# Kernel tuning notes

Hardware: AMD Instinct MI355X
Metric: run time of the kernel (lower is better)

Reference implementation:

```python
import jax, jax.numpy as jnp
import numpy as np

TOPK = 3
RAT_S = 0.05


def conv4d(x, w, bs):
    """Faithful fused version of the looped Conv4d (stride=1, padding=1, l_k=3).

    x:  (b, c_in, l, d, h, w)
    w:  (c_out, c_in, l_k, d_k, h_k, w_k)  -- w[:, :, i] is the i-th Conv3d weight
    bs: (l_k, c_out)                        -- per-i Conv3d biases
    The torch loop computes out[f] = sum_i conv3d_i(x[f + i - l_k//2]) for valid
    frame indices, which is exactly a 4D cross-correlation; the bias of conv3d_i
    is added once per VALID i, so boundary frames get fewer bias terms.
    """
    out = jax.lax.conv_general_dilated(
        x, w, window_strides=(1, 1, 1, 1), padding=[(1, 1)] * 4,
        dimension_numbers=("NCABXY", "OIABXY", "NCABXY"))
    l_i = x.shape[2]
    l_k = w.shape[2]
    f = jnp.arange(l_i)
    j = f[:, None] + jnp.arange(l_k)[None, :] - l_k // 2  # source frame per (f, i)
    valid = ((j >= 0) & (j < l_i)).astype(x.dtype)        # (l, l_k)
    bias = valid @ bs                                     # (l, c_out)
    return out + bias.T[None, :, :, None, None, None]


def zero_window(x_aff, h, w, rat_s):
    """x_aff: (b, h*w, h, w). Suppress a Gaussian window centered at each
    channel's (r, c) source location."""
    dt = x_aff.dtype
    sr = jnp.asarray(h * rat_s, dt)
    sc = jnp.asarray(w * rat_s, dt)
    ind_r = jnp.arange(h, dtype=dt)
    ind_c = jnp.arange(w, dtype=dt)
    cent_r = jnp.repeat(jnp.arange(h), w).astype(dt)  # (h*w,)
    cent_c = jnp.tile(jnp.arange(w), h).astype(dt)    # (h*w,)
    gr = jnp.exp(-((ind_r[None, :] - cent_r[:, None]) ** 2) / (2 * sr ** 2))  # (hw, h)
    gc = jnp.exp(-((ind_c[None, :] - cent_c[:, None]) ** 2) / (2 * sc ** 2))  # (hw, w)
    g = 1.0 - gr[:, :, None] * gc[:, None, :]  # (hw, h, w)
    return x_aff * g[None]


def setup_inputs() -> dict:
    key = jax.random.key(0)
    k = jax.random.split(key, 5)
    b, c, h, w = 4, 256, 32, 32
    x = jax.random.normal(k[0], (b, c, h, w), dtype=jnp.float32)
    w1 = jax.random.normal(k[1], (16, 1, 3, 3, 3, 3), dtype=jnp.float32) * 0.2
    b1 = jax.random.normal(k[2], (3, 16), dtype=jnp.float32) * 0.05
    w2 = jax.random.normal(k[3], (1, 16, 3, 3, 3, 3), dtype=jnp.float32) * 0.1
    b2 = jax.random.normal(k[4], (3, 1), dtype=jnp.float32) * 0.05
    return {"x": x, "w1": w1, "b1": b1, "w2": w2, "b2": b2}


def reference(x, w1, b1, w2, b2):
    b, c, h1, ww1 = x.shape
    n = h1 * ww1
    # F.normalize over channel dim (p=2, eps=1e-12)
    xn = x / jnp.maximum(jnp.linalg.norm(x, axis=1, keepdims=True), 1e-12)
    q = xn.transpose(0, 2, 3, 1).reshape(b, n, c)      # (b, hw, c)
    kmat = xn.reshape(b, c, n)                          # (b, c, hw)
    aff = jnp.einsum("bnc,bcm->bnm", q, kmat)          # (b, hw, hw)
    aff = zero_window(aff.reshape(b, n, h1, ww1), h1, ww1, RAT_S)
    x_fc = aff.reshape(b, 1, h1, ww1, h1, ww1)
    y = conv4d(x_fc, w1, b1)                            # (b, 16, h1, w1, h2, w2)
    y = conv4d(y, w2, b2)                               # (b, 1,  h1, w1, h2, w2)
    xc = y.reshape(b, n, h1, ww1)                       # (b, hw, h2, w2)
    # top-k values along dim=-3 (the query/channel axis)
    vals = jax.lax.top_k(xc.transpose(0, 2, 3, 1), TOPK)[0]  # (b, h2, w2, k)
    return vals.transpose(0, 3, 1, 2)                   # (b, k, h2, w2)
```

## Files before the change

kernel.cpp:

```cpp
#include <hip/hip_runtime.h>

#define HW 1024
#define CCH 256


typedef _Float16 h2v __attribute__((ext_vector_type(2)));
typedef short bf16x8 __attribute__((ext_vector_type(8)));
typedef float f32x4 __attribute__((ext_vector_type(4)));

__device__ __forceinline__ float fdot2(unsigned a, unsigned b, float c) {
#if __has_builtin(__builtin_amdgcn_fdot2)
    return __builtin_amdgcn_fdot2(__builtin_bit_cast(h2v, a),
                                  __builtin_bit_cast(h2v, b), c, false);
#else
    h2v ha = __builtin_bit_cast(h2v, a), hb = __builtin_bit_cast(h2v, b);
    return c + (float)ha.x * (float)hb.x + (float)ha.y * (float)hb.y;
#endif
}
__device__ __forceinline__ unsigned packh2(float x, float y) {
    h2v h;
    h.x = (_Float16)x;
    h.y = (_Float16)y;
    return __builtin_bit_cast(unsigned, h);
}
__device__ __forceinline__ unsigned short f2bf(float f) {
    unsigned u = __float_as_uint(f);
    u += 0x7fffu + ((u >> 16) & 1u);
    return (unsigned short)(u >> 16);
}

__global__ __launch_bounds__(256) void norm_kernel(const float* __restrict__ x,
                                                   unsigned short* __restrict__ xnT) {
    __shared__ float red[16][17];
    __shared__ float invs[16];
    int b = blockIdx.y;
    int p0 = blockIdx.x * 16;
    int cg = threadIdx.x >> 4;
    int pp = threadIdx.x & 15;
    int p = p0 + pp;
    const float* xb = x + (size_t)b * CCH * HW;
    float ss = 0.f;
#pragma unroll
    for (int i = 0; i < 16; ++i) {
        float v = xb[(size_t)(cg * 16 + i) * HW + p];
        ss += v * v;
    }
    red[cg][pp] = ss;
    __syncthreads();
    if (threadIdx.x < 16) {
        float s = 0.f;
#pragma unroll
        for (int g = 0; g < 16; ++g) s += red[g][threadIdx.x];
        invs[threadIdx.x] = 1.0f / fmaxf(sqrtf(s), 1e-12f);
    }
    __syncthreads();
    float inv = invs[pp];
    unsigned* o = (unsigned*)(xnT + ((size_t)b * HW + p) * CCH) + cg * 8;
#pragma unroll
    for (int i = 0; i < 8; ++i) {
        int c = cg * 16 + 2 * i;
        unsigned lo = f2bf(xb[(size_t)c * HW + p] * inv);
        unsigned hi = f2bf(xb[(size_t)(c + 1) * HW + p] * inv);
        o[i] = lo | (hi << 16);
    }
}

__global__ __launch_bounds__(256) void aff_kernel(const unsigned short* __restrict__ xnT,
                                                  unsigned short* __restrict__ Af16) {
    int b = blockIdx.z;
    int p0 = blockIdx.y * 64, m0 = blockIdx.x * 64;
    const unsigned short* X = xnT + (size_t)b * HW * CCH;
    int lane = threadIdx.x & 63, w = threadIdx.x >> 6;
    int pw = p0 + (w >> 1) * 32, mw = m0 + (w & 1) * 32;
    int lr = lane & 15, lg = lane >> 4;
    f32x4 acc[2][2] = {};
    for (int ks = 0; ks < 8; ++ks) {
        int kc = ks * 32 + lg * 8;
        bf16x8 a0 = *(const bf16x8*)&X[(size_t)(pw + lr) * CCH + kc];
        bf16x8 a1 = *(const bf16x8*)&X[(size_t)(pw + 16 + lr) * CCH + kc];
        bf16x8 b0 = *(const bf16x8*)&X[(size_t)(mw + lr) * CCH + kc];
        bf16x8 b1 = *(const bf16x8*)&X[(size_t)(mw + 16 + lr) * CCH + kc];
        acc[0][0] = __builtin_amdgcn_mfma_f32_16x16x32_bf16(a0, b0, acc[0][0], 0, 0, 0);
        acc[0][1] = __builtin_amdgcn_mfma_f32_16x16x32_bf16(a0, b1, acc[0][1], 0, 0, 0);
        acc[1][0] = __builtin_amdgcn_mfma_f32_16x16x32_bf16(a1, b0, acc[1][0], 0, 0, 0);
        acc[1][1] = __builtin_amdgcn_mfma_f32_16x16x32_bf16(a1, b1, acc[1][1], 0, 0, 0);
    }
#pragma unroll
    for (int pi = 0; pi < 2; ++pi)
#pragma unroll
        for (int mi = 0; mi < 2; ++mi)
#pragma unroll
            for (int r = 0; r < 4; ++r) {
                int p = pw + 16 * pi + lg * 4 + r;
                int m = mw + 16 * mi + lr;
                int dr = (m >> 5) - (p >> 5);
                int dc = (m & 31) - (p & 31);
                float gg = 1.0f - __expf(-(float)(dr * dr + dc * dc) * 0.1953125f);
                float v = acc[pi][mi][r] * gg;
                Af16[((size_t)b * HW + p) * HW + m] =
                    __builtin_bit_cast(unsigned short, (_Float16)v);
            }
}

__global__ __launch_bounds__(256) void g_kernel(const float* __restrict__ w1,
                                                const float* __restrict__ w2,
                                                float* __restrict__ G) {
    __shared__ float w1s[1296], w2s[1296];
    int tid = threadIdx.x;
    for (int i = tid; i < 1296; i += 256) { w1s[i] = w1[i]; w2s[i] = w2[i]; }
    __syncthreads();
    int idx = blockIdx.x * 256 + tid;
    if (idx < 6561) {
        int o1 = idx / 81, o2 = idx - o1 * 81;
        float s = 0.f;
#pragma unroll
        for (int ch = 0; ch < 16; ++ch) s += w1s[ch * 81 + o1] * w2s[ch * 81 + o2];
        G[idx] = s;
    }
}

__global__ __launch_bounds__(128) void wcomp_kernel(const float* __restrict__ G,
                                                    unsigned* __restrict__ Wpk) {
    __shared__ float Gs[6561];
    int cls = blockIdx.x;
    int t = threadIdx.x;
    for (int i = t; i < 6561; i += 128) Gs[i] = G[i];
    if (t < 25) Wpk[cls * 400 + t * 16 + 15] = 0u;
    __syncthreads();
    if (t >= 125) return;
    int a = t / 25, b_ = (t / 5) % 5, c = t % 5;
    int r1c = cls / 27, c1c = (cls / 9) % 3, r2c = (cls / 3) % 3, c2c = cls % 3;
    float W[5] = {};
    for (int i2 = 0; i2 < 3; ++i2) {
        if ((r1c == 0 && i2 == 0) || (r1c == 2 && i2 == 2)) continue;
        int i1 = a - i2;
        if (i1 < 0 || i1 > 2) continue;
        for (int j2 = 0; j2 < 3; ++j2) {
            if ((c1c == 0 && j2 == 0) || (c1c == 2 && j2 == 2)) continue;
            int j1 = b_ - j2;
            if (j1 < 0 || j1 > 2) continue;
            for (int u2 = 0; u2 < 3; ++u2) {
                if ((r2c == 0 && u2 == 0) || (r2c == 2 && u2 == 2)) continue;
                int u1 = c - u2;
                if (u1 < 0 || u1 > 2) continue;
                for (int v2 = 0; v2 < 3; ++v2) {
                    if ((c2c == 0 && v2 == 0) || (c2c == 2 && v2 == 2)) continue;
                    int o2 = i2 * 27 + j2 * 9 + u2 * 3 + v2;
                    int o1b = i1 * 27 + j1 * 9 + u1 * 3;
#pragma unroll
                    for (int d = 0; d < 5; ++d) {
                        int v1 = d - v2;
                        if (v1 < 0 || v1 > 2) continue;
                        W[d] += Gs[(o1b + v1) * 81 + o2];
                    }
                }
            }
        }
    }
    unsigned* o = &Wpk[cls * 400 + (a * 5 + b_) * 16 + c * 3];
    o[0] = packh2(W[0], W[1]);
    o[1] = packh2(W[2], W[3]);
    o[2] = packh2(W[4], 0.f);
}

__global__ __launch_bounds__(1024) void bt_kernel(const float* __restrict__ w2,
                                                  const float* __restrict__ b1,
                                                  const float* __restrict__ b2,
                                                  float* __restrict__ BT) {
    __shared__ float w2s[1296], b1s[48], S0[81], S1[81], S2[81];
    int t = threadIdx.x;
    for (int i = t; i < 1296; i += 1024) w2s[i] = w2[i];
    if (t < 48) b1s[t] = b1[t];
    __syncthreads();
    if (t < 81) {
        float s0 = 0.f, s1 = 0.f, s2 = 0.f;
#pragma unroll
        for (int ch = 0; ch < 16; ++ch) {
            float w = w2s[ch * 81 + t];
            s0 += w * b1s[16 + ch];
            s1 += w * b1s[ch];
            s2 += w * b1s[32 + ch];
        }
        S0[t] = s0; S1[t] = s1; S2[t] = s2;
    }
    __syncthreads();
    if (t >= 864) return;
    int r1 = t / 27, c1c = (t / 9) % 3, r2c = (t / 3) % 3, c2c = t % 3;
    float s = b2[1] + (r1 >= 1 ? b2[0] : 0.f) + (r1 <= 30 ? b2[2] : 0.f);
    for (int i2 = 0; i2 < 3; ++i2) {
        int rr = r1 + i2 - 1;
        if (rr < 0 || rr > 31) continue;
        float m1 = (rr >= 1) ? 1.f : 0.f, m2 = (rr <= 30) ? 1.f : 0.f;
        for (int j2 = 0; j2 < 3; ++j2) {
            if ((c1c == 0 && j2 == 0) || (c1c == 2 && j2 == 2)) continue;
            for (int u2 = 0; u2 < 3; ++u2) {
                if ((r2c == 0 && u2 == 0) || (r2c == 2 && u2 == 2)) continue;
                for (int v2 = 0; v2 < 3; ++v2) {
                    if ((c2c == 0 && v2 == 0) || (c2c == 2 && v2 == 2)) continue;
                    int o2 = i2 * 27 + j2 * 9 + u2 * 3 + v2;
                    s += S0[o2] + m1 * S1[o2] + m2 * S2[o2];
                }
            }
        }
    }
    BT[t] = s;
}

#define HS 80
__global__ __launch_bounds__(256) void convc_kernel(const unsigned short* __restrict__ Af16,
                                                    const unsigned* __restrict__ Wpk,
                                                    const float* __restrict__ BT,
                                                    float* __restrict__ xc) {
    __shared__ unsigned short halo[2][36 * HS];
    int tid = threadIdx.x;
    int P = blockIdx.x, b = blockIdx.y;
    int r1 = P >> 5, c1 = P & 31;
    int r1c = (r1 == 0) ? 0 : (r1 == 31) ? 2 : 1;
    int c1c = (c1 == 0) ? 0 : (c1 == 31) ? 2 : 1;

    const uint4* wsrc = (const uint4*)(Wpk + (size_t)((r1c * 3 + c1c) * 9 + 4) * 400);
    float bias = BT[r1 * 27 + c1c * 9 + 4];

    for (int i = tid; i < 36 * HS; i += 256) ((unsigned*)halo)[i] = 0;

    int qr = tid >> 3, qc = tid & 7;
    int dstw = (qr + 2) * 40 + 2 * qc + 1;
    const uint2* Ab = (const uint2*)(Af16 + (size_t)b * HW * HW);

    float acc0 = 0.f, acc1 = 0.f, acc2 = 0.f, acc3 = 0.f;

    int pr0 = min(max(r1 - 2, 0), 31), pc0 = min(max(c1 - 2, 0), 31);
    uint2 pf = Ab[(size_t)(pr0 * 32 + pc0) * 256 + tid];

    __syncthreads();
    int buf = 0;

#pragma unroll 1
    for (int tp = 0; tp < 25; ++tp) {
        int tr = tp / 5, tc = tp - tr * 5;
        int apr = r1 + tr - 2, apc = c1 + tc - 2;
        bool valid = ((unsigned)apr < 32u) && ((unsigned)apc < 32u);
        uint2 cur = pf;
        if (tp < 24) {
            int t2 = tp + 1;
            int tr2 = t2 / 5, tc2 = t2 - tr2 * 5;
            int npr = min(max(r1 + tr2 - 2, 0), 31);
            int npc = min(max(c1 + tc2 - 2, 0), 31);
            pf = Ab[(size_t)(npr * 32 + npc) * 256 + tid];
        }
        if (!valid) continue;

        uint4 w4a = wsrc[tp * 4 + 0];
        uint4 w4b = wsrc[tp * 4 + 1];
        uint4 w4c = wsrc[tp * 4 + 2];
        uint4 w4d = wsrc[tp * 4 + 3];

        unsigned* hb = (unsigned*)halo[buf];
        hb[dstw] = cur.x;
        hb[dstw + 1] = cur.y;
        __syncthreads();

        unsigned wr[16] = {w4a.x, w4a.y, w4a.z, w4a.w, w4b.x, w4b.y, w4b.z, w4b.w,
                           w4c.x, w4c.y, w4c.z, w4c.w, w4d.x, w4d.y, w4d.z, w4d.w};
        const unsigned* hbr = (const unsigned*)halo[buf];
#pragma unroll
        for (int u = 0; u < 5; ++u) {
            const unsigned* dp = hbr + (qr + u) * 40 + 2 * qc;
            uint2 d01 = *(const uint2*)dp;
            uint2 d23 = *(const uint2*)(dp + 2);
            unsigned u4v = dp[4];
            unsigned u0 = d01.x, u1v = d01.y, u2v = d23.x, u3v = d23.y;
            unsigned o0 = (u0 >> 16) | (u1v << 16);
            unsigned o1 = (u1v >> 16) | (u2v << 16);
            unsigned o2 = (u2v >> 16) | (u3v << 16);
            unsigned o3 = (u3v >> 16) | (u4v << 16);
            acc0 = fdot2(wr[u * 3 + 0], u0, acc0);
            acc0 = fdot2(wr[u * 3 + 1], u1v, acc0);
            acc0 = fdot2(wr[u * 3 + 2], u2v, acc0);
            acc1 = fdot2(wr[u * 3 + 0], o0, acc1);
            acc1 = fdot2(wr[u * 3 + 1], o1, acc1);
            acc1 = fdot2(wr[u * 3 + 2], o2, acc1);
            acc2 = fdot2(wr[u * 3 + 0], u1v, acc2);
            acc2 = fdot2(wr[u * 3 + 1], u2v, acc2);
            acc2 = fdot2(wr[u * 3 + 2], u3v, acc2);
            acc3 = fdot2(wr[u * 3 + 0], o1, acc3);
            acc3 = fdot2(wr[u * 3 + 1], o2, acc3);
            acc3 = fdot2(wr[u * 3 + 2], o3, acc3);
        }
        buf ^= 1;
    }

    float4 res = make_float4(acc0 + bias, acc1 + bias, acc2 + bias, acc3 + bias);
    *(float4*)&xc[((size_t)b * HW + P) * HW + qr * 32 + 4 * qc] = res;
}

__global__ __launch_bounds__(256) void expand_kernel(const unsigned short* __restrict__ Af16,
                                                     unsigned* __restrict__ Apad32) {
    int plane = blockIdx.x, b = blockIdx.y;
    const unsigned* src = (const unsigned*)(Af16 + ((size_t)b * HW + plane) * HW);
    unsigned* dst = Apad32 + ((size_t)b * HW + plane) * 720;
    for (int k = threadIdx.x; k < 720; k += 256) {
        int pr = k / 20, pcd = k - pr * 20;
        unsigned val = 0;
        if (pr >= 2 && pr < 34 && pcd >= 1 && pcd <= 16)
            val = src[(pr - 2) * 16 + (pcd - 1)];
        dst[k] = val;
    }
}

__global__ __launch_bounds__(128) void fix_kernel(const unsigned* __restrict__ Apad32,
                                                  const unsigned* __restrict__ Wpk,
                                                  const float* __restrict__ BT,
                                                  float* __restrict__ xc) {
    __shared__ __align__(16) unsigned wl[3600];
    __shared__ float bts[9];
    int tid = threadIdx.x;
    int P = blockIdx.x, b = blockIdx.y;
    int r1 = P >> 5, c1 = P & 31;
    int r1c = (r1 == 0) ? 0 : (r1 == 31) ? 2 : 1;
    int c1c = (c1 == 0) ? 0 : (c1 == 31) ? 2 : 1;

    const unsigned* wsrc = Wpk + (size_t)(r1c * 3 + c1c) * 3600;
    for (int i = tid; i < 3600; i += 128) wl[i] = wsrc[i];
    if (tid < 9) bts[tid] = BT[r1 * 27 + c1c * 9 + tid];

    int li = tid;
    bool act = li < 124;
    int qr, qc;
    if (li < 32) { qr = 0; qc = li; }
    else if (li < 64) { qr = 31; qc = li - 32; }
    else if (li < 94) { qr = li - 63; qc = 0; }
    else { qr = min(li, 123) - 93; qc = 31; }
    int r2c = (qr == 0) ? 0 : (qr == 31) ? 2 : 1;
    int c2c = (qc == 0) ? 0 : (qc == 31) ? 2 : 1;
    int v = r2c * 3 + c2c;
    int sh = (qc & 1) * 16;
    int sd = qc >> 1;

    __syncthreads();
    float acc = 0.f;

#pragma unroll 1
    for (int tp = 0; tp < 25; ++tp) {
        int tr = tp / 5, tc = tp - tr * 5;
        int apr = r1 + tr - 2, apc = c1 + tc - 2;
        if ((unsigned)apr >= 32u || (unsigned)apc >= 32u) continue;
        const unsigned* tpl = Apad32 + ((size_t)b * HW + apr * 32 + apc) * 720;
        const uint4* wv4 = (const uint4*)&wl[v * 400 + tp * 16];
        uint4 wa = wv4[0], wb = wv4[1], wc2 = wv4[2], wd = wv4[3];
        unsigned wr[16] = {wa.x, wa.y, wa.z, wa.w, wb.x, wb.y, wb.z, wb.w,
                           wc2.x, wc2.y, wc2.z, wc2.w, wd.x, wd.y, wd.z, wd.w};
#pragma unroll
        for (int u = 0; u < 5; ++u) {
            const unsigned* rp = tpl + (qr + u) * 20 + sd;
            unsigned d0 = rp[0], d1 = rp[1], d2 = rp[2];
            unsigned pa = __builtin_amdgcn_alignbit(d1, d0, sh);
            unsigned pb = __builtin_amdgcn_alignbit(d2, d1, sh);
            unsigned pc_ = __builtin_amdgcn_alignbit(0u, d2, sh);
            acc = fdot2(wr[u * 3 + 0], pa, acc);
            acc = fdot2(wr[u * 3 + 1], pb, acc);
            acc = fdot2(wr[u * 3 + 2], pc_, acc);
        }
    }

    if (act)
        xc[((size_t)b * HW + P) * HW + qr * 32 + qc] = acc + bts[v];
}

__device__ __forceinline__ void top3_push(float v, float& t0, float& t1, float& t2) {
    float n0 = fminf(t0, v);
    t0 = fmaxf(t0, v);
    float n1 = fminf(t1, n0);
    t1 = fmaxf(t1, n0);
    t2 = fmaxf(t2, n1);
}

__global__ __launch_bounds__(256) void topk1_kernel(const float* __restrict__ xc,
                                                    float* __restrict__ part) {
    int q = blockIdx.x * 256 + threadIdx.x;
    int pc = blockIdx.y, bi = blockIdx.z;
    float t0 = -1e30f, t1 = -1e30f, t2 = -1e30f;
    const float* xp = xc + (size_t)bi * HW * HW;
    for (int p = pc * 32; p < pc * 32 + 32; ++p)
        top3_push(xp[(size_t)p * HW + q], t0, t1, t2);
    float* pp = part + (size_t)(bi * 32 + pc) * 3 * HW;
    pp[q] = t0;
    pp[HW + q] = t1;
    pp[2 * HW + q] = t2;
}

__global__ __launch_bounds__(256) void topk2_kernel(const float* __restrict__ part,
                                                    float* __restrict__ out) {
    int q = blockIdx.x * 256 + threadIdx.x;
    int bi = blockIdx.y;
    float t0 = -1e30f, t1 = -1e30f, t2 = -1e30f;
    const float* pp = part + (size_t)bi * 96 * HW;
    for (int k = 0; k < 96; ++k) top3_push(pp[(size_t)k * HW + q], t0, t1, t2);
    float* ob = out + (size_t)bi * 3 * HW;
    ob[q] = t0;
    ob[HW + q] = t1;
    ob[2 * HW + q] = t2;
}

extern "C" void kernel_launch(void* const* d_in, const int* in_sizes, int n_in,
                              void* d_out, int out_size, void* d_ws, size_t ws_size,
                              hipStream_t stream) {
    const float* x = (const float*)d_in[0];
    const float* w1 = (const float*)d_in[1];
    const float* b1 = (const float*)d_in[2];
    const float* w2 = (const float*)d_in[3];
    const float* b2 = (const float*)d_in[4];
    float* out = (float*)d_out;
    float* ws = (float*)d_ws;

    unsigned short* xnT = (unsigned short*)ws;
    unsigned short* Af16 = (unsigned short*)(ws + 524288);
    float* xc = ws + 2621440;
    unsigned* Wpk = (unsigned*)(ws + 6815744);
    float* BT = ws + 6848512;
    float* part = ws + 6849536;
    unsigned* Apad32 = (unsigned*)(ws + 7242752);
    float* G = ws + 10191872;

    norm_kernel<<<dim3(64, 4), 256, 0, stream>>>(x, xnT);
    aff_kernel<<<dim3(16, 16, 4), 256, 0, stream>>>(xnT, Af16);
    expand_kernel<<<dim3(1024, 4), 256, 0, stream>>>(Af16, Apad32);
    g_kernel<<<26, 256, 0, stream>>>(w1, w2, G);
    wcomp_kernel<<<81, 128, 0, stream>>>(G, Wpk);
    bt_kernel<<<1, 1024, 0, stream>>>(w2, b1, b2, BT);
    convc_kernel<<<dim3(1024, 4), 256, 0, stream>>>(Af16, Wpk, BT, xc);
    fix_kernel<<<dim3(1024, 4), 128, 0, stream>>>(Apad32, Wpk, BT, xc);
    topk1_kernel<<<dim3(4, 32, 4), 256, 0, stream>>>(xc, part);
    topk2_kernel<<<dim3(4, 4), 256, 0, stream>>>(part, out);
}
```

Baseline: 184.8 us.

## Register-block convc outputs to 16 per thread with 64-thread blocks

```diff
diff --git a/kernel.cpp b/kernel.cpp
--- a/kernel.cpp
+++ b/kernel.cpp
@@ -206,12 +206,12 @@
     BT[t] = s;
 }
 
-#define HS 80
-__global__ __launch_bounds__(256) void convc_kernel(const unsigned short* __restrict__ Af16,
-                                                    const unsigned* __restrict__ Wpk,
-                                                    const float* __restrict__ BT,
-                                                    float* __restrict__ xc) {
-    __shared__ unsigned short halo[2][36 * HS];
+#define HSD 56
+__global__ __launch_bounds__(64) void convc_kernel(const unsigned short* __restrict__ Af16,
+                                                   const unsigned* __restrict__ Wpk,
+                                                   const float* __restrict__ BT,
+                                                   float* __restrict__ xc) {
+    __shared__ unsigned halo[36 * HSD];
     int tid = threadIdx.x;
     int P = blockIdx.x, b = blockIdx.y;
     int r1 = P >> 5, c1 = P & 31;
@@ -221,32 +221,37 @@
     const uint4* wsrc = (const uint4*)(Wpk + (size_t)((r1c * 3 + c1c) * 9 + 4) * 400);
     float bias = BT[r1 * 27 + c1c * 9 + 4];
 
-    for (int i = tid; i < 36 * HS; i += 256) ((unsigned*)halo)[i] = 0;
-
-    int qr = tid >> 3, qc = tid & 7;
-    int dstw = (qr + 2) * 40 + 2 * qc + 1;
-    const uint2* Ab = (const uint2*)(Af16 + (size_t)b * HW * HW);
-
-    float acc0 = 0.f, acc1 = 0.f, acc2 = 0.f, acc3 = 0.f;
+    for (int i = tid; i < 36 * HSD; i += 64) halo[i] = 0;
+
+    int qr2 = tid >> 2;
+    int qc = tid & 3;
+    int srow = tid >> 1;
+    int st = tid & 1;
+    int wbase = (srow + 2) * HSD + 8 * st + 1;
+
+    const uint4* Ab4 = (const uint4*)(Af16 + (size_t)b * HW * HW);
+
+    float acc0[8] = {}, acc1[8] = {};
 
     int pr0 = min(max(r1 - 2, 0), 31), pc0 = min(max(c1 - 2, 0), 31);
-    uint2 pf = Ab[(size_t)(pr0 * 32 + pc0) * 256 + tid];
-
-    __syncthreads();
-    int buf = 0;
+    uint4 pfA = Ab4[(size_t)(pr0 * 32 + pc0) * 128 + 2 * tid];
+    uint4 pfB = Ab4[(size_t)(pr0 * 32 + pc0) * 128 + 2 * tid + 1];
+
+    __syncthreads();
 
 #pragma unroll 1
     for (int tp = 0; tp < 25; ++tp) {
         int tr = tp / 5, tc = tp - tr * 5;
         int apr = r1 + tr - 2, apc = c1 + tc - 2;
         bool valid = ((unsigned)apr < 32u) && ((unsigned)apc < 32u);
-        uint2 cur = pf;
+        uint4 curA = pfA, curB = pfB;
         if (tp < 24) {
             int t2 = tp + 1;
             int tr2 = t2 / 5, tc2 = t2 - tr2 * 5;
             int npr = min(max(r1 + tr2 - 2, 0), 31);
             int npc = min(max(c1 + tc2 - 2, 0), 31);
-            pf = Ab[(size_t)(npr * 32 + npc) * 256 + tid];
+            pfA = Ab4[(size_t)(npr * 32 + npc) * 128 + 2 * tid];
+            pfB = Ab4[(size_t)(npr * 32 + npc) * 128 + 2 * tid + 1];
         }
         if (!valid) continue;
 
@@ -255,43 +260,65 @@
         uint4 w4c = wsrc[tp * 4 + 2];
         uint4 w4d = wsrc[tp * 4 + 3];
 
-        unsigned* hb = (unsigned*)halo[buf];
-        hb[dstw] = cur.x;
-        hb[dstw + 1] = cur.y;
+        __syncthreads();
+        {
+            unsigned* hb = &halo[wbase];
+            hb[0] = curA.x; hb[1] = curA.y; hb[2] = curA.z; hb[3] = curA.w;
+            hb[4] = curB.x; hb[5] = curB.y; hb[6] = curB.z; hb[7] = curB.w;
+        }
         __syncthreads();
 
         unsigned wr[16] = {w4a.x, w4a.y, w4a.z, w4a.w, w4b.x, w4b.y, w4b.z, w4b.w,
                            w4c.x, w4c.y, w4c.z, w4c.w, w4d.x, w4d.y, w4d.z, w4d.w};
-        const unsigned* hbr = (const unsigned*)halo[buf];
-#pragma unroll
-        for (int u = 0; u < 5; ++u) {
-            const unsigned* dp = hbr + (qr + u) * 40 + 2 * qc;
-            uint2 d01 = *(const uint2*)dp;
-            uint2 d23 = *(const uint2*)(dp + 2);
-            unsigned u4v = dp[4];
-            unsigned u0 = d01.x, u1v = d01.y, u2v = d23.x, u3v = d23.y;
-            unsigned o0 = (u0 >> 16) | (u1v << 16);
-            unsigned o1 = (u1v >> 16) | (u2v << 16);
-            unsigned o2 = (u2v >> 16) | (u3v << 16);
-            unsigned o3 = (u3v >> 16) | (u4v << 16);
-            acc0 = fdot2(wr[u * 3 + 0], u0, acc0);
-            acc0 = fdot2(wr[u * 3 + 1], u1v, acc0);
-            acc0 = fdot2(wr[u * 3 + 2], u2v, acc0);
-            acc1 = fdot2(wr[u * 3 + 0], o0, acc1);
-            acc1 = fdot2(wr[u * 3 + 1], o1, acc1);
-            acc1 = fdot2(wr[u * 3 + 2], o2, acc1);
-            acc2 = fdot2(wr[u * 3 + 0], u1v, acc2);
-            acc2 = fdot2(wr[u * 3 + 1], u2v, acc2);
-            acc2 = fdot2(wr[u * 3 + 2], u3v, acc2);
-            acc3 = fdot2(wr[u * 3 + 0], o1, acc3);
-            acc3 = fdot2(wr[u * 3 + 1], o2, acc3);
-            acc3 = fdot2(wr[u * 3 + 2], o3, acc3);
-        }
-        buf ^= 1;
-    }
-
-    float4 res = make_float4(acc0 + bias, acc1 + bias, acc2 + bias, acc3 + bias);
-    *(float4*)&xc[((size_t)b * HW + P) * HW + qr * 32 + 4 * qc] = res;
+        const unsigned* base = &halo[(2 * qr2) * HSD + 4 * qc];
+#pragma unroll
+        for (int i = 0; i < 6; ++i) {
+            const unsigned* rp = base + i * HSD;
+            uint2 e0 = *(const uint2*)rp;
+            uint2 e1 = *(const uint2*)(rp + 2);
+            uint2 e2 = *(const uint2*)(rp + 4);
+            unsigned q0 = e0.x, q1 = e0.y, q2 = e1.x, q3 = e1.y, q4 = e2.x, q5 = e2.y;
+            unsigned pp[12];
+            pp[0] = q0;  pp[2] = q1;  pp[4] = q2;  pp[6] = q3;  pp[8] = q4;  pp[10] = q5;
+            pp[1] = (q0 >> 16) | (q1 << 16);
+            pp[3] = (q1 >> 16) | (q2 << 16);
+            pp[5] = (q2 >> 16) | (q3 << 16);
+            pp[7] = (q3 >> 16) | (q4 << 16);
+            pp[9] = (q4 >> 16) | (q5 << 16);
+            pp[11] = (q5 >> 16);
+            if (i <= 4) {
+                unsigned wa = wr[i * 3], wb_ = wr[i * 3 + 1], wc_ = wr[i * 3 + 2];
+#pragma unroll
+                for (int cc = 0; cc < 8; ++cc) {
+                    float a = acc0[cc];
+                    a = fdot2(wa, pp[cc], a);
+                    a = fdot2(wb_, pp[cc + 2], a);
+                    a = fdot2(wc_, pp[cc + 4], a);
+                    acc0[cc] = a;
+                }
+            }
+            if (i >= 1) {
+                int u = i - 1;
+                unsigned wa = wr[u * 3], wb_ = wr[u * 3 + 1], wc_ = wr[u * 3 + 2];
+#pragma unroll
+                for (int cc = 0; cc < 8; ++cc) {
+                    float a = acc1[cc];
+                    a = fdot2(wa, pp[cc], a);
+                    a = fdot2(wb_, pp[cc + 2], a);
+                    a = fdot2(wc_, pp[cc + 4], a);
+                    acc1[cc] = a;
+                }
+            }
+        }
+    }
+
+    float* xp = &xc[((size_t)b * HW + P) * HW];
+    int o0 = (2 * qr2) * 32 + 8 * qc;
+    int o1 = (2 * qr2 + 1) * 32 + 8 * qc;
+    *(float4*)&xp[o0] = make_float4(acc0[0] + bias, acc0[1] + bias, acc0[2] + bias, acc0[3] + bias);
+    *(float4*)&xp[o0 + 4] = make_float4(acc0[4] + bias, acc0[5] + bias, acc0[6] + bias, acc0[7] + bias);
+    *(float4*)&xp[o1] = make_float4(acc1[0] + bias, acc1[1] + bias, acc1[2] + bias, acc1[3] + bias);
+    *(float4*)&xp[o1 + 4] = make_float4(acc1[4] + bias, acc1[5] + bias, acc1[6] + bias, acc1[7] + bias);
 }
 
 __global__ __launch_bounds__(256) void expand_kernel(const unsigned short* __restrict__ Af16,
@@ -428,7 +455,7 @@
     g_kernel<<<26, 256, 0, stream>>>(w1, w2, G);
     wcomp_kernel<<<81, 128, 0, stream>>>(G, Wpk);
     bt_kernel<<<1, 1024, 0, stream>>>(w2, b1, b2, BT);
-    convc_kernel<<<dim3(1024, 4), 256, 0, stream>>>(Af16, Wpk, BT, xc);
+    convc_kernel<<<dim3(1024, 4), 64, 0, stream>>>(Af16, Wpk, BT, xc);
     fix_kernel<<<dim3(1024, 4), 128, 0, stream>>>(Apad32, Wpk, BT, xc);
     topk1_kernel<<<dim3(4, 32, 4), 256, 0, stream>>>(xc, part);
     topk2_kernel<<<dim3(4, 4), 256, 0, stream>>>(part, out);
```

Result: faster. 178.0 us (-3.7%).

## Recast fused 4D conv as MFMA matmul over outer taps plus inner shift-add

Applied to the files above, without the earlier changes.

```diff
diff --git a/kernel.cpp b/kernel.cpp
--- a/kernel.cpp
+++ b/kernel.cpp
@@ -5,6 +5,7 @@
 
 
 typedef _Float16 h2v __attribute__((ext_vector_type(2)));
+typedef _Float16 f16x8 __attribute__((ext_vector_type(8)));
 typedef short bf16x8 __attribute__((ext_vector_type(8)));
 typedef float f32x4 __attribute__((ext_vector_type(4)));
 
@@ -27,6 +28,12 @@
     unsigned u = __float_as_uint(f);
     u += 0x7fffu + ((u >> 16) & 1u);
     return (unsigned short)(u >> 16);
+}
+__device__ __forceinline__ unsigned short f2h(float f) {
+    return __builtin_bit_cast(unsigned short, (_Float16)f);
+}
+__device__ __forceinline__ float h2f(unsigned short u) {
+    return (float)__builtin_bit_cast(_Float16, u);
 }
 
 __global__ __launch_bounds__(256) void norm_kernel(const float* __restrict__ x,
@@ -120,12 +127,21 @@
 }
 
 __global__ __launch_bounds__(128) void wcomp_kernel(const float* __restrict__ G,
-                                                    unsigned* __restrict__ Wpk) {
+                                                    unsigned* __restrict__ Wpk,
+                                                    unsigned short* __restrict__ Wmf) {
     __shared__ float Gs[6561];
     int cls = blockIdx.x;
     int t = threadIdx.x;
     for (int i = t; i < 6561; i += 128) Gs[i] = G[i];
     if (t < 25) Wpk[cls * 400 + t * 16 + 15] = 0u;
+    bool emit = (cls % 9) == 4;
+    unsigned short* wm = Wmf + (size_t)(cls / 9) * 1024;
+    if (emit) {
+        for (int i = t; i < 1024; i += 128) {
+            int m = i >> 5, k = i & 31;
+            if (m >= 25 || k >= 25) wm[i] = 0;
+        }
+    }
     __syncthreads();
     if (t >= 125) return;
     int a = t / 25, b_ = (t / 5) % 5, c = t % 5;
@@ -161,6 +177,11 @@
     o[0] = packh2(W[0], W[1]);
     o[1] = packh2(W[2], W[3]);
     o[2] = packh2(W[4], 0.f);
+    if (emit) {
+        int k = a * 5 + b_;
+#pragma unroll
+        for (int d = 0; d < 5; ++d) wm[(c * 5 + d) * 32 + k] = f2h(W[d]);
+    }
 }
 
 __global__ __launch_bounds__(1024) void bt_kernel(const float* __restrict__ w2,
@@ -206,92 +227,98 @@
     BT[t] = s;
 }
 
-#define HS 80
 __global__ __launch_bounds__(256) void convc_kernel(const unsigned short* __restrict__ Af16,
-                                                    const unsigned* __restrict__ Wpk,
+                                                    const unsigned short* __restrict__ Wmf,
                                                     const float* __restrict__ BT,
                                                     float* __restrict__ xc) {
-    __shared__ unsigned short halo[2][36 * HS];
+    __shared__ __align__(16) unsigned short S[32768];
     int tid = threadIdx.x;
+    int w = tid >> 6, lane = tid & 63;
     int P = blockIdx.x, b = blockIdx.y;
     int r1 = P >> 5, c1 = P & 31;
     int r1c = (r1 == 0) ? 0 : (r1 == 31) ? 2 : 1;
     int c1c = (c1 == 0) ? 0 : (c1 == 31) ? 2 : 1;
-
-    const uint4* wsrc = (const uint4*)(Wpk + (size_t)((r1c * 3 + c1c) * 9 + 4) * 400);
+    int cls9 = r1c * 3 + c1c;
     float bias = BT[r1 * 27 + c1c * 9 + 4];
 
-    for (int i = tid; i < 36 * HS; i += 256) ((unsigned*)halo)[i] = 0;
-
-    int qr = tid >> 3, qc = tid & 7;
-    int dstw = (qr + 2) * 40 + 2 * qc + 1;
-    const uint2* Ab = (const uint2*)(Af16 + (size_t)b * HW * HW);
-
-    float acc0 = 0.f, acc1 = 0.f, acc2 = 0.f, acc3 = 0.f;
-
-    int pr0 = min(max(r1 - 2, 0), 31), pc0 = min(max(c1 - 2, 0), 31);
-    uint2 pf = Ab[(size_t)(pr0 * 32 + pc0) * 256 + tid];
-
-    __syncthreads();
-    int buf = 0;
-
-#pragma unroll 1
-    for (int tp = 0; tp < 25; ++tp) {
-        int tr = tp / 5, tc = tp - tr * 5;
-        int apr = r1 + tr - 2, apc = c1 + tc - 2;
-        bool valid = ((unsigned)apr < 32u) && ((unsigned)apc < 32u);
-        uint2 cur = pf;
-        if (tp < 24) {
-            int t2 = tp + 1;
-            int tr2 = t2 / 5, tc2 = t2 - tr2 * 5;
-            int npr = min(max(r1 + tr2 - 2, 0), 31);
-            int npc = min(max(c1 + tc2 - 2, 0), 31);
-            pf = Ab[(size_t)(npr * 32 + npc) * 256 + tid];
-        }
-        if (!valid) continue;
-
-        uint4 w4a = wsrc[tp * 4 + 0];
-        uint4 w4b = wsrc[tp * 4 + 1];
-        uint4 w4c = wsrc[tp * 4 + 2];
-        uint4 w4d = wsrc[tp * 4 + 3];
-
-        unsigned* hb = (unsigned*)halo[buf];
-        hb[dstw] = cur.x;
-        hb[dstw + 1] = cur.y;
-        __syncthreads();
-
-        unsigned wr[16] = {w4a.x, w4a.y, w4a.z, w4a.w, w4b.x, w4b.y, w4b.z, w4b.w,
-                           w4c.x, w4c.y, w4c.z, w4c.w, w4d.x, w4d.y, w4d.z, w4d.w};
-        const unsigned* hbr = (const unsigned*)halo[buf];
+    {
+        uint4* S4 = (uint4*)S;
+        for (int i = tid; i < 4096; i += 256) S4[i] = make_uint4(0, 0, 0, 0);
+    }
+    __syncthreads();
+
+    for (int i = tid; i < 25 * 128; i += 256) {
+        int dp = i >> 7, chunk = i & 127;
+        int tr = dp / 5, tc = dp - tr * 5;
+        int pr = r1 + tr - 2, pc = c1 + tc - 2;
+        if (((unsigned)pr < 32u) && ((unsigned)pc < 32u)) {
+            uint4 v = *(const uint4*)&Af16[((size_t)b * HW + pr * 32 + pc) * HW + chunk * 8];
+            int kg = dp >> 3;
+            int qx = (chunk * 8) ^ (kg << 4);
+            *(uint4*)&S[dp * 1024 + qx] = v;
+        }
+    }
+
+    const unsigned short* wm = Wmf + (size_t)cls9 * 1024;
+    int lr = lane & 15, kg2 = lane >> 4;
+    f16x8 a0 = *(const f16x8*)&wm[lr * 32 + kg2 * 8];
+    f16x8 a1 = *(const f16x8*)&wm[(16 + lr) * 32 + kg2 * 8];
+
+    __syncthreads();
+
+    f32x4 acc0[16], acc1[16];
+    int xsh = kg2 << 4;
+#pragma unroll
+    for (int nt = 0; nt < 16; ++nt) {
+        int q = w * 256 + nt * 16 + lr;
+        int qq = q ^ xsh;
+        const unsigned short* col = &S[kg2 * 8 * 1024 + qq];
+        f16x8 bf;
+#pragma unroll
+        for (int j = 0; j < 8; ++j)
+            bf[j] = __builtin_bit_cast(_Float16, col[j * 1024]);
+        f32x4 z = {0.f, 0.f, 0.f, 0.f};
+        acc0[nt] = __builtin_amdgcn_mfma_f32_16x16x32_f16(a0, bf, z, 0, 0, 0);
+        acc1[nt] = __builtin_amdgcn_mfma_f32_16x16x32_f16(a1, bf, z, 0, 0, 0);
+    }
+
+    __syncthreads();
+
+#pragma unroll
+    for (int nt = 0; nt < 16; ++nt) {
+        int q = w * 256 + nt * 16 + lr;
+        int tb = kg2 * 4;
+#pragma unroll
+        for (int r = 0; r < 4; ++r) {
+            S[(tb + r) * 1040 + q] = f2h(acc0[nt][r]);
+            int t1 = 16 + tb + r;
+            if (t1 < 25) S[t1 * 1040 + q] = f2h(acc1[nt][r]);
+        }
+    }
+    __syncthreads();
+
+    float* xp = &xc[((size_t)b * HW + P) * HW];
+#pragma unroll
+    for (int k = 0; k < 4; ++k) {
+        int q = tid + 256 * k;
+        int qr = q >> 5, qc = q & 31;
+        float s = bias;
 #pragma unroll
         for (int u = 0; u < 5; ++u) {
-            const unsigned* dp = hbr + (qr + u) * 40 + 2 * qc;
-            uint2 d01 = *(const uint2*)dp;
-            uint2 d23 = *(const uint2*)(dp + 2);
-            unsigned u4v = dp[4];
-            unsigned u0 = d01.x, u1v = d01.y, u2v = d23.x, u3v = d23.y;
-            unsigned o0 = (u0 >> 16) | (u1v << 16);
-            unsigned o1 = (u1v >> 16) | (u2v << 16);
-            unsigned o2 = (u2v >> 16) | (u3v << 16);
-            unsigned o3 = (u3v >> 16) | (u4v << 16);
-            acc0 = fdot2(wr[u * 3 + 0], u0, acc0);
-            acc0 = fdot2(wr[u * 3 + 1], u1v, acc0);
-            acc0 = fdot2(wr[u * 3 + 2], u2v, acc0);
-            acc1 = fdot2(wr[u * 3 + 0], o0, acc1);
-            acc1 = fdot2(wr[u * 3 + 1], o1, acc1);
-            acc1 = fdot2(wr[u * 3 + 2], o2, acc1);
-            acc2 = fdot2(wr[u * 3 + 0], u1v, acc2);
-            acc2 = fdot2(wr[u * 3 + 1], u2v, acc2);
-            acc2 = fdot2(wr[u * 3 + 2], u3v, acc2);
-            acc3 = fdot2(wr[u * 3 + 0], o1, acc3);
-            acc3 = fdot2(wr[u * 3 + 1], o2, acc3);
-            acc3 = fdot2(wr[u * 3 + 2], o3, acc3);
-        }
-        buf ^= 1;
-    }
-
-    float4 res = make_float4(acc0 + bias, acc1 + bias, acc2 + bias, acc3 + bias);
-    *(float4*)&xc[((size_t)b * HW + P) * HW + qr * 32 + 4 * qc] = res;
+            int rr = qr + u - 2;
+            bool rv = ((unsigned)rr < 32u);
+            int rbase = rr * 32;
+#pragma unroll
+            for (int v = 0; v < 5; ++v) {
+                int cc = qc + v - 2;
+                bool ok = rv && ((unsigned)cc < 32u);
+                int idx = ok ? ((u * 5 + v) * 1040 + rbase + cc) : 0;
+                float val = h2f(S[idx]);
+                s += ok ? val : 0.f;
+            }
+        }
+        xp[q] = s;
+    }
 }
 
 __global__ __launch_bounds__(256) void expand_kernel(const unsigned short* __restrict__ Af16,
@@ -421,14 +448,15 @@
     float* part = ws + 6849536;
     unsigned* Apad32 = (unsigned*)(ws + 7242752);
     float* G = ws + 10191872;
+    unsigned short* Wmf = (unsigned short*)(ws + 10198440);
 
     norm_kernel<<<dim3(64, 4), 256, 0, stream>>>(x, xnT);
     aff_kernel<<<dim3(16, 16, 4), 256, 0, stream>>>(xnT, Af16);
     expand_kernel<<<dim3(1024, 4), 256, 0, stream>>>(Af16, Apad32);
     g_kernel<<<26, 256, 0, stream>>>(w1, w2, G);
-    wcomp_kernel<<<81, 128, 0, stream>>>(G, Wpk);
+    wcomp_kernel<<<81, 128, 0, stream>>>(G, Wpk, Wmf);
     bt_kernel<<<1, 1024, 0, stream>>>(w2, b1, b2, BT);
-    convc_kernel<<<dim3(1024, 4), 256, 0, stream>>>(Af16, Wpk, BT, xc);
+    convc_kernel<<<dim3(1024, 4), 256, 0, stream>>>(Af16, Wmf, BT, xc);
     fix_kernel<<<dim3(1024, 4), 128, 0, stream>>>(Apad32, Wpk, BT, xc);
     topk1_kernel<<<dim3(4, 32, 4), 256, 0, stream>>>(xc, part);
     topk2_kernel<<<dim3(4, 4), 256, 0, stream>>>(part, out);
```

New measurement: 191.8 us. 3.8% more time.
